# Performance work log

Hardware: AMD Instinct MI355X
Metric: run time of the kernel (lower is better)

## Reference

```python
import jax, jax.numpy as jnp
import numpy as np

B, S, H, A = 16, 2048, 1024, 8


def setup_inputs() -> dict:
    key = jax.random.key(0)
    k1, k2, k3, k4 = jax.random.split(key, 4)
    token_embeddings = jax.random.normal(k1, (B, S, H), dtype=jnp.float32)
    aspect_embedding = jax.random.normal(k2, (B, A, H), dtype=jnp.float32)
    # Linear(2H -> H): stored as [2H, H] so we can use x @ W (same math as torch W^T)
    W = jax.random.normal(k3, (2 * H, H), dtype=jnp.float32) * (1.0 / np.sqrt(2 * H))
    b = jnp.zeros((H,), dtype=jnp.float32)
    v = jax.random.uniform(k4, (H,), dtype=jnp.float32)  # torch.rand init
    return {"token_embeddings": token_embeddings, "aspect_embedding": aspect_embedding,
            "W": W, "b": b, "v": v}


def reference(token_embeddings, aspect_embedding, W, b, v):
    # mean-pool aspect tokens -> [B, 1, H], broadcast over seq
    asp = jnp.mean(aspect_embedding, axis=1, keepdims=True)
    asp = jnp.broadcast_to(asp, token_embeddings.shape)          # [B, S, H]
    combined = jnp.concatenate([token_embeddings, asp], axis=2)   # [B, S, 2H]
    energy = jnp.tanh(combined @ W + b)                           # [B, S, H]
    scores = jnp.einsum('bsh,h->bs', energy, v)                   # [B, S]
    weights = jax.nn.softmax(scores, axis=1)                      # [B, S]
    # token * weights + token  ==  token * (1 + weights)
    return token_embeddings * (1.0 + weights[:, :, None])
```

## Files before the change

kernel.cpp:

```cpp
#include <hip/hip_runtime.h>
#include <hip/hip_bf16.h>
#include <stdint.h>


#define SEQ 2048
#define H 1024
#define MTOT 32768
#define BK 32

typedef __bf16 bf16x8 __attribute__((ext_vector_type(8)));
typedef float  f32x4  __attribute__((ext_vector_type(4)));

__device__ __forceinline__ void async16(const void* g, void* l) {
  __builtin_amdgcn_global_load_lds(
      (const __attribute__((address_space(1))) unsigned*)g,
      (__attribute__((address_space(3))) unsigned*)l, 16, 0, 0);
}

__device__ __forceinline__ unsigned f2bfraw(float f) {
  unsigned x = __float_as_uint(f);
  return (x + 0x7fffu + ((x >> 16) & 1u)) >> 16;
}
__device__ __forceinline__ float fast_tanh(float x) {
  x = fminf(fmaxf(x, -40.0f), 40.0f);
  float e = __expf(2.0f * x);
  return 1.0f - 2.0f / (e + 1.0f);
}

__global__ __launch_bounds__(256) void prep_all(
    const float* __restrict__ W,
    const float* __restrict__ asp,
    const float* __restrict__ bias,
    const float* __restrict__ tok,
    unsigned short* __restrict__ WT,
    float* __restrict__ cpart,
    unsigned short* __restrict__ tokb) {
  __shared__ __align__(16) float shbuf[1312];
  const int t = threadIdx.x;
  if (blockIdx.x >= 1280) {
    size_t i = ((size_t)(blockIdx.x - 1280) * 256 + t) * 8;
    const size_t stride = (size_t)2048 * 256 * 8;
#pragma unroll
    for (int it = 0; it < 8; ++it, i += stride) {
      const f32x4 a = *reinterpret_cast<const f32x4*>(tok + i);
      const f32x4 b = *reinterpret_cast<const f32x4*>(tok + i + 4);
      uint4 r;
      r.x = f2bfraw(a[0]) | (f2bfraw(a[1]) << 16);
      r.y = f2bfraw(a[2]) | (f2bfraw(a[3]) << 16);
      r.z = f2bfraw(b[0]) | (f2bfraw(b[1]) << 16);
      r.w = f2bfraw(b[2]) | (f2bfraw(b[3]) << 16);
      *reinterpret_cast<uint4*>(tokb + i) = r;
    }
  } else if (blockIdx.x < 1024) {
    float (*tile)[33] = reinterpret_cast<float(*)[33]>(shbuf);
    const int x = t & 31, y = t >> 5;
    const int n0 = (blockIdx.x & 31) * 32, k0 = (blockIdx.x >> 5) * 32;
#pragma unroll
    for (int i = 0; i < 4; ++i)
      tile[y + 8 * i][x] = W[(size_t)(k0 + y + 8 * i) * H + n0 + x];
    __syncthreads();
#pragma unroll
    for (int i = 0; i < 4; ++i)
      WT[(size_t)(n0 + y + 8 * i) * H + k0 + x] =
          (unsigned short)f2bfraw(tile[x][y + 8 * i]);
  } else {
    const int idx = blockIdx.x - 1024;
    const int b = idx & 15, nc = (idx >> 4) & 3, kc = idx >> 6;
    const int lane = t & 63, w = t >> 6;
    float* am = shbuf;
    f32x4* red = reinterpret_cast<f32x4*>(shbuf + 256);
    {
      const int k = kc * 256 + t;
      float s = 0.f;
#pragma unroll
      for (int a = 0; a < 8; ++a) s += asp[(size_t)(b * 8 + a) * H + k];
      am[t] = s * 0.125f;
    }
    __syncthreads();
    const int n = nc * 256 + lane * 4;
    const float* wp = W + (size_t)(H + kc * 256 + w * 64) * H + n;
    f32x4 acc = {};
#pragma unroll 8
    for (int k = 0; k < 64; ++k) {
      const f32x4 wv = *reinterpret_cast<const f32x4*>(wp + (size_t)k * H);
      const float a = am[w * 64 + k];
      acc[0] += a * wv[0]; acc[1] += a * wv[1];
      acc[2] += a * wv[2]; acc[3] += a * wv[3];
    }
    red[w * 64 + lane] = acc;
    __syncthreads();
    if (w == 0) {
      f32x4 r = red[lane];
#pragma unroll
      for (int i = 1; i < 4; ++i) {
        const f32x4 x = red[i * 64 + lane];
        r[0] += x[0]; r[1] += x[1]; r[2] += x[2]; r[3] += x[3];
      }
      if (kc == 0) {
        r[0] += bias[n];     r[1] += bias[n + 1];
        r[2] += bias[n + 2]; r[3] += bias[n + 3];
      }
      *reinterpret_cast<f32x4*>(cpart + (size_t)kc * 16 * H + b * H + n) = r;
    }
  }
}

__global__ __launch_bounds__(512) void gemm_score(
    const __hip_bfloat16* __restrict__ tokb,
    const __hip_bfloat16* __restrict__ wt,
    const float* __restrict__ cpart,
    const float* __restrict__ v,
    float* __restrict__ part) {
  __shared__ __hip_bfloat16 lds[2 * 12288];
  const int t = threadIdx.x;
  const int lane = t & 63;
  const int w = t >> 6;
  const int wm = w >> 1, wn = w & 1;
  const unsigned bidl = blockIdx.x + (blockIdx.y << 3);
  const unsigned nb = ((bidl & 7u) << 7) | (bidl >> 3);
  const int bx = nb & 7;
  const int by = nb >> 3;
  const int m0 = by * 256;
  const int n0 = bx * 128;
  const int bb = by >> 3;

  f32x4 acc[4][4] = {};

  const int srow = t >> 2;
  const int scol = 8 * ((t & 3) ^ ((t >> 3) & 3));
  const __hip_bfloat16* ga = tokb + (size_t)(m0 + srow) * H + scol;
  const __hip_bfloat16* gb = wt + (size_t)(n0 + srow) * H + scol;
  const int quad = lane >> 4, l16 = lane & 15;
  const int sq = quad ^ ((l16 >> 1) & 3);

  auto stage = [&](int kt, int buf) {
    __hip_bfloat16* p = lds + buf * 12288 + t * 8;
    const int off = kt * BK;
    async16(ga + off, p);
    async16(ga + off + (size_t)128 * H, p + 4096);
    async16(gb + off, p + 8192);
  };
  auto compute = [&](int buf) {
    const __hip_bfloat16* As = lds + buf * 12288;
    const __hip_bfloat16* Bs = As + 8192;
    bf16x8 af[4], bf[4];
#pragma unroll
    for (int mi = 0; mi < 4; ++mi)
      af[mi] = *reinterpret_cast<const bf16x8*>(
          As + (wm * 64 + mi * 16 + l16) * BK + sq * 8);
#pragma unroll
    for (int ni = 0; ni < 4; ++ni)
      bf[ni] = *reinterpret_cast<const bf16x8*>(
          Bs + (wn * 64 + ni * 16 + l16) * BK + sq * 8);
#pragma unroll
    for (int mi = 0; mi < 4; ++mi)
#pragma unroll
      for (int ni = 0; ni < 4; ++ni)
        acc[mi][ni] = __builtin_amdgcn_mfma_f32_16x16x32_bf16(
            af[mi], bf[ni], acc[mi][ni], 0, 0, 0);
  };

  stage(0, 0);
  int cur = 0;
  for (int kt = 0; kt < 32; ++kt) {
    __syncthreads();
    if (kt + 1 < 32) stage(kt + 1, cur ^ 1);
    compute(cur);
    cur ^= 1;
  }

  float vv[4], cc[4];
#pragma unroll
  for (int ni = 0; ni < 4; ++ni) {
    const int gn = n0 + wn * 64 + ni * 16 + l16;
    vv[ni] = v[gn];
    float s = cpart[(size_t)bb * H + gn];
    s += cpart[(size_t)1 * 16 * H + bb * H + gn];
    s += cpart[(size_t)2 * 16 * H + bb * H + gn];
    s += cpart[(size_t)3 * 16 * H + bb * H + gn];
    cc[ni] = s;
  }
  const size_t pbase = ((size_t)bx * 2 + wn) * MTOT + m0;
#pragma unroll
  for (int mi = 0; mi < 4; ++mi) {
#pragma unroll
    for (int r = 0; r < 4; ++r) {
      float s = 0.f;
#pragma unroll
      for (int ni = 0; ni < 4; ++ni)
        s += fast_tanh(acc[mi][ni][r] + cc[ni]) * vv[ni];
#pragma unroll
      for (int msk = 1; msk < 16; msk <<= 1) s += __shfl_xor(s, msk, 64);
      if (l16 == 0)
        part[pbase + wm * 64 + mi * 16 + quad * 4 + r] = s;
    }
  }
}

__global__ __launch_bounds__(1024) void softmax_k(
    const float* __restrict__ part, float* __restrict__ wts) {
  const int b = blockIdx.x, t = threadIdx.x;
  const int lane = t & 63, w = t >> 6;
  __shared__ float red[16];
  const int s0 = t * 2;
  float sx = 0.f, sy = 0.f;
#pragma unroll
  for (int p = 0; p < 16; ++p) {
    const float2 x = *reinterpret_cast<const float2*>(
        part + (size_t)p * MTOT + b * SEQ + s0);
    sx += x.x; sy += x.y;
  }
  float m = fmaxf(sx, sy);
#pragma unroll
  for (int o = 1; o < 64; o <<= 1) m = fmaxf(m, __shfl_xor(m, o, 64));
  if (lane == 0) red[w] = m;
  __syncthreads();
  m = red[0];
#pragma unroll
  for (int i = 1; i < 16; ++i) m = fmaxf(m, red[i]);
  __syncthreads();
  const float e0 = __expf(sx - m), e1 = __expf(sy - m);
  float sum = e0 + e1;
#pragma unroll
  for (int o = 1; o < 64; o <<= 1) sum += __shfl_xor(sum, o, 64);
  if (lane == 0) red[w] = sum;
  __syncthreads();
  sum = 0.f;
#pragma unroll
  for (int i = 0; i < 16; ++i) sum += red[i];
  const float inv = 1.0f / sum;
  float2 o2; o2.x = e0 * inv; o2.y = e1 * inv;
  *reinterpret_cast<float2*>(wts + (size_t)b * SEQ + s0) = o2;
}

__global__ __launch_bounds__(256) void scale_k(
    const float* __restrict__ tok, const float* __restrict__ wts,
    float* __restrict__ out) {
  size_t i = ((size_t)blockIdx.x * 256 + threadIdx.x) * 4;
  const size_t stride = (size_t)2048 * 256 * 4;
#pragma unroll
  for (int it = 0; it < 16; ++it, i += stride) {
    const float wm = 1.0f + wts[i >> 10];
    const f32x4 a = *reinterpret_cast<const f32x4*>(tok + i);
    f32x4 o;
    o[0] = a[0] * wm; o[1] = a[1] * wm; o[2] = a[2] * wm; o[3] = a[3] * wm;
    *reinterpret_cast<f32x4*>(out + i) = o;
  }
}

extern "C" void kernel_launch(void* const* d_in, const int* in_sizes, int n_in,
                              void* d_out, int out_size, void* d_ws, size_t ws_size,
                              hipStream_t stream) {
  const float* tok  = (const float*)d_in[0];
  const float* asp  = (const float*)d_in[1];
  const float* W    = (const float*)d_in[2];
  const float* bias = (const float*)d_in[3];
  const float* v    = (const float*)d_in[4];
  float* out = (float*)d_out;

  unsigned short* tokb_u = (unsigned short*)out;
  float*          cpart  = out + 16777216;
  float*          part   = out + 32505856;
  unsigned short* WT_u   = (unsigned short*)(out + 33030144);
  float* wts = (ws_size >= (size_t)(SEQ * 16 * 4)) ? (float*)d_ws
                                                   : (float*)d_in[1];

  prep_all<<<3328, 256, 0, stream>>>(W, asp, bias, tok, WT_u, cpart, tokb_u);
  gemm_score<<<dim3(8, 128), 512, 0, stream>>>(
      (const __hip_bfloat16*)tokb_u, (const __hip_bfloat16*)WT_u,
      cpart, v, part);
  softmax_k<<<16, 1024, 0, stream>>>(part, wts);
  scale_k<<<2048, 256, 0, stream>>>(tok, wts, out);
}
```

Measured before the change: 372.7 us.

## Fuse fp32-to-bf16 token conversion into GEMM LDS stage, drop prepass

The separate prep pass that converted the 64MB fp32 token tensor to bf16 is removed. The GEMM now async-loads fp32 token tiles straight into LDS with an XOR swizzle and converts them to bf16 in registers just before the MFMA. This saves a full read of tokens plus a write and re-read of the bf16 copy, at the cost of twice the A-tile LDS traffic, more LDS per block (80KB) and conversion ALU work inside the inner loop. The scale kernel is also flattened to one vector per thread with a 16x larger grid.

```diff
diff --git a/kernel.cpp b/kernel.cpp
--- a/kernel.cpp
+++ b/kernel.cpp
@@ -7,6 +7,7 @@
 #define H 1024
 #define MTOT 32768
 #define BK 32
+#define LDSBUF 40960
 
 typedef __bf16 bf16x8 __attribute__((ext_vector_type(8)));
 typedef float  f32x4  __attribute__((ext_vector_type(4)));
@@ -31,27 +32,11 @@
     const float* __restrict__ W,
     const float* __restrict__ asp,
     const float* __restrict__ bias,
-    const float* __restrict__ tok,
     unsigned short* __restrict__ WT,
-    float* __restrict__ cpart,
-    unsigned short* __restrict__ tokb) {
+    float* __restrict__ cpart) {
   __shared__ __align__(16) float shbuf[1312];
   const int t = threadIdx.x;
-  if (blockIdx.x >= 1280) {
-    size_t i = ((size_t)(blockIdx.x - 1280) * 256 + t) * 8;
-    const size_t stride = (size_t)2048 * 256 * 8;
-#pragma unroll
-    for (int it = 0; it < 8; ++it, i += stride) {
-      const f32x4 a = *reinterpret_cast<const f32x4*>(tok + i);
-      const f32x4 b = *reinterpret_cast<const f32x4*>(tok + i + 4);
-      uint4 r;
-      r.x = f2bfraw(a[0]) | (f2bfraw(a[1]) << 16);
-      r.y = f2bfraw(a[2]) | (f2bfraw(a[3]) << 16);
-      r.z = f2bfraw(b[0]) | (f2bfraw(b[1]) << 16);
-      r.w = f2bfraw(b[2]) | (f2bfraw(b[3]) << 16);
-      *reinterpret_cast<uint4*>(tokb + i) = r;
-    }
-  } else if (blockIdx.x < 1024) {
+  if (blockIdx.x < 1024) {
     float (*tile)[33] = reinterpret_cast<float(*)[33]>(shbuf);
     const int x = t & 31, y = t >> 5;
     const int n0 = (blockIdx.x & 31) * 32, k0 = (blockIdx.x >> 5) * 32;
@@ -106,12 +91,12 @@
 }
 
 __global__ __launch_bounds__(512) void gemm_score(
-    const __hip_bfloat16* __restrict__ tokb,
+    const float* __restrict__ tokf,
     const __hip_bfloat16* __restrict__ wt,
     const float* __restrict__ cpart,
     const float* __restrict__ v,
     float* __restrict__ part) {
-  __shared__ __hip_bfloat16 lds[2 * 12288];
+  __shared__ __align__(16) unsigned char smem[2 * LDSBUF];
   const int t = threadIdx.x;
   const int lane = t & 63;
   const int w = t >> 6;
@@ -126,32 +111,49 @@
 
   f32x4 acc[4][4] = {};
 
-  const int srow = t >> 2;
-  const int scol = 8 * ((t & 3) ^ ((t >> 3) & 3));
-  const __hip_bfloat16* ga = tokb + (size_t)(m0 + srow) * H + scol;
-  const __hip_bfloat16* gb = wt + (size_t)(n0 + srow) * H + scol;
+  const int arow = t >> 3;
+  const int acol = ((t & 7) ^ (arow & 7)) * 4;
+  const float* ga = tokf + (size_t)(m0 + arow) * H + acol;
+  const int brow = t >> 2;
+  const int bcol = ((t & 3) ^ (brow & 3)) * 8;
+  const __hip_bfloat16* gb = wt + (size_t)(n0 + brow) * H + bcol;
   const int quad = lane >> 4, l16 = lane & 15;
-  const int sq = quad ^ ((l16 >> 1) & 3);
 
   auto stage = [&](int kt, int buf) {
-    __hip_bfloat16* p = lds + buf * 12288 + t * 8;
+    float* Af = reinterpret_cast<float*>(smem + buf * LDSBUF);
+    __hip_bfloat16* Bs =
+        reinterpret_cast<__hip_bfloat16*>(smem + buf * LDSBUF + 32768);
     const int off = kt * BK;
-    async16(ga + off, p);
-    async16(ga + off + (size_t)128 * H, p + 4096);
-    async16(gb + off, p + 8192);
+#pragma unroll
+    for (int it = 0; it < 4; ++it)
+      async16(ga + off + (size_t)(it * 64) * H, Af + (it * 512 + t) * 4);
+    async16(gb + off, Bs + t * 8);
   };
   auto compute = [&](int buf) {
-    const __hip_bfloat16* As = lds + buf * 12288;
-    const __hip_bfloat16* Bs = As + 8192;
+    const float* Af = reinterpret_cast<const float*>(smem + buf * LDSBUF);
+    const __hip_bfloat16* Bs =
+        reinterpret_cast<const __hip_bfloat16*>(smem + buf * LDSBUF + 32768);
     bf16x8 af[4], bf[4];
 #pragma unroll
-    for (int mi = 0; mi < 4; ++mi)
-      af[mi] = *reinterpret_cast<const bf16x8*>(
-          As + (wm * 64 + mi * 16 + l16) * BK + sq * 8);
-#pragma unroll
-    for (int ni = 0; ni < 4; ++ni)
-      bf[ni] = *reinterpret_cast<const bf16x8*>(
-          Bs + (wn * 64 + ni * 16 + l16) * BK + sq * 8);
+    for (int mi = 0; mi < 4; ++mi) {
+      const int rA = wm * 64 + mi * 16 + l16;
+      const int s0 = (2 * quad) ^ (rA & 7);
+      const f32x4 flo = *reinterpret_cast<const f32x4*>(Af + rA * 32 + s0 * 4);
+      const f32x4 fhi =
+          *reinterpret_cast<const f32x4*>(Af + rA * 32 + (s0 ^ 1) * 4);
+      bf16x8 a;
+      a[0] = (__bf16)flo[0]; a[1] = (__bf16)flo[1];
+      a[2] = (__bf16)flo[2]; a[3] = (__bf16)flo[3];
+      a[4] = (__bf16)fhi[0]; a[5] = (__bf16)fhi[1];
+      a[6] = (__bf16)fhi[2]; a[7] = (__bf16)fhi[3];
+      af[mi] = a;
+    }
+#pragma unroll
+    for (int ni = 0; ni < 4; ++ni) {
+      const int rB = wn * 64 + ni * 16 + l16;
+      const int sq = quad ^ (rB & 3);
+      bf[ni] = *reinterpret_cast<const bf16x8*>(Bs + rB * 32 + sq * 8);
+    }
 #pragma unroll
     for (int mi = 0; mi < 4; ++mi)
 #pragma unroll
@@ -236,16 +238,12 @@
 __global__ __launch_bounds__(256) void scale_k(
     const float* __restrict__ tok, const float* __restrict__ wts,
     float* __restrict__ out) {
-  size_t i = ((size_t)blockIdx.x * 256 + threadIdx.x) * 4;
-  const size_t stride = (size_t)2048 * 256 * 4;
-#pragma unroll
-  for (int it = 0; it < 16; ++it, i += stride) {
-    const float wm = 1.0f + wts[i >> 10];
-    const f32x4 a = *reinterpret_cast<const f32x4*>(tok + i);
-    f32x4 o;
-    o[0] = a[0] * wm; o[1] = a[1] * wm; o[2] = a[2] * wm; o[3] = a[3] * wm;
-    *reinterpret_cast<f32x4*>(out + i) = o;
-  }
+  const size_t i = ((size_t)blockIdx.x * 256 + threadIdx.x) * 4;
+  const float wm = 1.0f + wts[i >> 10];
+  const f32x4 a = *reinterpret_cast<const f32x4*>(tok + i);
+  f32x4 o;
+  o[0] = a[0] * wm; o[1] = a[1] * wm; o[2] = a[2] * wm; o[3] = a[3] * wm;
+  *reinterpret_cast<f32x4*>(out + i) = o;
 }
 
 extern "C" void kernel_launch(void* const* d_in, const int* in_sizes, int n_in,
@@ -258,17 +256,15 @@
   const float* v    = (const float*)d_in[4];
   float* out = (float*)d_out;
 
-  unsigned short* tokb_u = (unsigned short*)out;
   float*          cpart  = out + 16777216;
   float*          part   = out + 32505856;
   unsigned short* WT_u   = (unsigned short*)(out + 33030144);
   float* wts = (ws_size >= (size_t)(SEQ * 16 * 4)) ? (float*)d_ws
                                                    : (float*)d_in[1];
 
-  prep_all<<<3328, 256, 0, stream>>>(W, asp, bias, tok, WT_u, cpart, tokb_u);
+  prep_all<<<1280, 256, 0, stream>>>(W, asp, bias, WT_u, cpart);
   gemm_score<<<dim3(8, 128), 512, 0, stream>>>(
-      (const __hip_bfloat16*)tokb_u, (const __hip_bfloat16*)WT_u,
-      cpart, v, part);
+      tok, (const __hip_bfloat16*)WT_u, cpart, v, part);
   softmax_k<<<16, 1024, 0, stream>>>(part, wts);
-  scale_k<<<2048, 256, 0, stream>>>(tok, wts, out);
-}
+  scale_k<<<32768, 256, 0, stream>>>(tok, wts, out);
+}
```

New measurement: 364.1 us. 2.3% less time.
